# Kernel optimization log

Measured on AMD Instinct MI355X. Metric: run time of the kernel, lower is better.

## Reference

```python
import jax, jax.numpy as jnp
import numpy as np

N = 50000
E = 800000
IN_C = 256
H1 = 64
H2 = 64
OUT_C = 32
HEADS = 7
NEG_SLOPE = 0.2


def _gat_layer(x, src, dst, W, a_src, a_dst, b, heads, ch, n_nodes):
    # x: [N, F_in]; W: [F_in, heads*ch]; a_src/a_dst: [heads, ch]; b: [heads*ch]
    h = (x @ W).reshape(n_nodes, heads, ch)                      # [N, H, C]
    alpha_s = jnp.einsum('nhc,hc->nh', h, a_src)                 # [N, H]
    alpha_d = jnp.einsum('nhc,hc->nh', h, a_dst)                 # [N, H]
    e = jax.nn.leaky_relu(alpha_s[src] + alpha_d[dst], NEG_SLOPE)  # [E, H]
    # segment softmax grouped by destination node
    m = jax.ops.segment_max(e, dst, num_segments=n_nodes)        # [N, H]
    e = jnp.exp(e - m[dst])
    denom = jax.ops.segment_sum(e, dst, num_segments=n_nodes)    # [N, H]
    alpha = e / (denom[dst] + 1e-16)                             # [E, H]
    msg = h[src] * alpha[:, :, None]                             # [E, H, C]
    out = jax.ops.segment_sum(msg, dst, num_segments=n_nodes)    # [N, H, C]
    return out.reshape(n_nodes, heads * ch) + b


def setup_inputs() -> dict:
    key = jax.random.key(0)
    ks = jax.random.split(key, 16)
    x = jax.random.normal(ks[0], (N, IN_C), dtype=jnp.float32)
    edge_index = jax.random.randint(ks[1], (2, E), 0, N, dtype=jnp.int32)

    def glorot(k, shape):
        fan = shape[0] + shape[-1]
        return jax.random.normal(k, shape, dtype=jnp.float32) * jnp.sqrt(2.0 / fan)

    W1 = glorot(ks[2], (IN_C, HEADS * H1))
    a1_src = glorot(ks[3], (HEADS, H1))
    a1_dst = glorot(ks[4], (HEADS, H1))
    b1 = jnp.zeros((HEADS * H1,), jnp.float32)

    W2 = glorot(ks[5], (HEADS * H1, HEADS * H2))
    a2_src = glorot(ks[6], (HEADS, H2))
    a2_dst = glorot(ks[7], (HEADS, H2))
    b2 = jnp.zeros((HEADS * H2,), jnp.float32)

    W3 = glorot(ks[8], (HEADS * H2, 1 * OUT_C))
    a3_src = glorot(ks[9], (1, OUT_C))
    a3_dst = glorot(ks[10], (1, OUT_C))
    b3 = jnp.zeros((OUT_C,), jnp.float32)

    return {"x": x, "edge_index": edge_index,
            "W1": W1, "a1_src": a1_src, "a1_dst": a1_dst, "b1": b1,
            "W2": W2, "a2_src": a2_src, "a2_dst": a2_dst, "b2": b2,
            "W3": W3, "a3_src": a3_src, "a3_dst": a3_dst, "b3": b3}


def reference(x, edge_index, W1, a1_src, a1_dst, b1, W2, a2_src, a2_dst, b2,
              W3, a3_src, a3_dst, b3):
    # PyG GATConv adds self-loops by default
    loops = jnp.arange(N, dtype=edge_index.dtype)
    src = jnp.concatenate([edge_index[0], loops])
    dst = jnp.concatenate([edge_index[1], loops])
    # dropout is identity in eval mode
    h = _gat_layer(x, src, dst, W1, a1_src, a1_dst, b1, HEADS, H1, N)
    h = jax.nn.relu(h)
    h = _gat_layer(h, src, dst, W2, a2_src, a2_dst, b2, HEADS, H2, N)
    h = jax.nn.relu(h)
    h = _gat_layer(h, src, dst, W3, a3_src, a3_dst, b3, 1, OUT_C, N)
    return jax.nn.log_softmax(h, axis=1)
```

## Files before the change

kernel.cpp:

```cpp
#include <hip/hip_runtime.h>
#include <hip/hip_bf16.h>
#include <hip/hip_fp16.h>

#define NN 50000
#define NP 50176
#define EE 800000
#define ET (EE + NN)
#define NB_SCAN ((NN + 255) / 256)

typedef __attribute__((ext_vector_type(8))) short bf16x8;
typedef __attribute__((ext_vector_type(4))) float f32x4;

static __device__ __forceinline__ float bf2f(__hip_bfloat16 x) { return __bfloat162float(x); }
static __device__ __forceinline__ ushort f2bu(float f) {
    union { __hip_bfloat16 b; ushort u; } c;
    c.b = __float2bfloat16(f);
    return c.u;
}
static __device__ __forceinline__ float u2f(ushort u) {
    union { ushort u; __hip_bfloat16 b; } c;
    c.u = u;
    return __bfloat162float(c.b);
}
static __device__ __forceinline__ unsigned char f2fp8(float v) {
    int p = __builtin_amdgcn_cvt_pk_fp8_f32(v, v, 0, false);
    return (unsigned char)(p & 0xff);
}
static __device__ __forceinline__ void fp8acc4(unsigned v, float w, float* acc) {
#if __has_builtin(__builtin_amdgcn_cvt_pk_f32_fp8)
    auto f01 = __builtin_amdgcn_cvt_pk_f32_fp8((int)v, false);
    auto f23 = __builtin_amdgcn_cvt_pk_f32_fp8((int)v, true);
    acc[0] += w * f01[0];
    acc[1] += w * f01[1];
    acc[2] += w * f23[0];
    acc[3] += w * f23[1];
#else
    acc[0] += w * __builtin_amdgcn_cvt_f32_fp8(v, 0);
    acc[1] += w * __builtin_amdgcn_cvt_f32_fp8(v, 1);
    acc[2] += w * __builtin_amdgcn_cvt_f32_fp8(v, 2);
    acc[3] += w * __builtin_amdgcn_cvt_f32_fp8(v, 3);
#endif
}
static __device__ __forceinline__ void gl2lds(const ushort* g, ushort* l) {
    __builtin_amdgcn_global_load_lds(
        (const __attribute__((address_space(1))) void*)g,
        (__attribute__((address_space(3))) void*)l,
        16, 0, 0);
}

#define PA1 (256 * 448)
#define PA2 (448 * 448)
#define PA3 (448 * 32)
#define PXQ (NN * 64)
#define PTOT (PA1 + PA2 + PA3 + PXQ)
#define PBLK ((PTOT + 255) / 256)
#define CBLK ((ET + 255) / 256)

__global__ void gat_prepcnt_kernel(const float* __restrict__ W1, const float* __restrict__ W2,
                                   const float* __restrict__ W3, const float* __restrict__ x,
                                   ushort* __restrict__ Wt1, ushort* __restrict__ Wt2,
                                   ushort* __restrict__ Wt3, ushort* __restrict__ xb,
                                   const int* __restrict__ ei, int* __restrict__ cnt) {
    int b = blockIdx.x;
    if (b >= PBLK) {
        int i = (b - PBLK) * 256 + threadIdx.x;
        if (i < ET) {
            int dst = (i < EE) ? ei[EE + i] : (i - EE);
            atomicAdd(&cnt[dst], 1);
        }
        return;
    }
    int i = b * 256 + threadIdx.x;
    if (i < PA1) {
        int k = i / 448, n = i - k * 448;
        Wt1[(size_t)n * 256 + k] = f2bu(W1[i]);
        return;
    }
    i -= PA1;
    if (i < PA2) {
        int k = i / 448, n = i - k * 448;
        Wt2[(size_t)n * 448 + k] = f2bu(W2[i]);
        return;
    }
    i -= PA2;
    if (i < PA3) {
        int k = i / 32, n = i - k * 32;
        Wt3[(size_t)n * 448 + k] = f2bu(W3[i]);
        return;
    }
    i -= PA3;
    if (i < PXQ) {
        float4 f = ((const float4*)x)[i];
        ushort u[4] = {f2bu(f.x), f2bu(f.y), f2bu(f.z), f2bu(f.w)};
        ((uint2*)xb)[i] = *(const uint2*)u;
    }
}

__global__ void gat_scan1_kernel(const int* __restrict__ cnt, int* __restrict__ tmp,
                                 int* __restrict__ part) {
    __shared__ int sm[256];
    int tid = threadIdx.x;
    int i = blockIdx.x * 256 + tid;
    int v = (i < NN) ? cnt[i] : 0;
    sm[tid] = v;
    __syncthreads();
    for (int o = 1; o < 256; o <<= 1) {
        int t = (tid >= o) ? sm[tid - o] : 0;
        __syncthreads();
        sm[tid] += t;
        __syncthreads();
    }
    if (i < NN) tmp[i] = sm[tid];
    if (tid == 255) part[blockIdx.x] = sm[255];
}

__global__ void gat_scan2_kernel(int* __restrict__ part) {
    __shared__ int sm[256];
    int tid = threadIdx.x;
    int v = (tid < NB_SCAN) ? part[tid] : 0;
    sm[tid] = v;
    __syncthreads();
    for (int o = 1; o < 256; o <<= 1) {
        int t = (tid >= o) ? sm[tid - o] : 0;
        __syncthreads();
        sm[tid] += t;
        __syncthreads();
    }
    part[tid] = sm[tid];
}

__global__ void gat_scan3_kernel(const int* __restrict__ tmp, const int* __restrict__ part,
                                 int* __restrict__ row_ptr) {
    int i = blockIdx.x * 256 + threadIdx.x;
    int off = (blockIdx.x > 0) ? part[blockIdx.x - 1] : 0;
    if (i < NN) row_ptr[i + 1] = tmp[i] + off;
    if (i == 0) row_ptr[0] = 0;
}

__global__ void gat_fill_kernel(const int* __restrict__ ei, const int* __restrict__ row_ptr,
                                int* __restrict__ fillc, int* __restrict__ colA) {
    int i = blockIdx.x * blockDim.x + threadIdx.x;
    if (i >= ET) return;
    int s, d;
    if (i < EE) { s = ei[i]; d = ei[EE + i]; }
    else        { s = d = i - EE; }
    int pos = row_ptr[d] + atomicAdd(&fillc[d], 1);
    colA[pos] = s;
}

#define GBN 64
#define GBK 32

template <int RF, int DOA, int OM>
__global__ __launch_bounds__(256) void gat_gemm_kernel(
    const ushort* __restrict__ A, const ushort* __restrict__ Wt,
    void* __restrict__ Cv,
    const float* __restrict__ Asrc, const float* __restrict__ Adst,
    float* __restrict__ as8, float* __restrict__ ad8,
    int M, int K, int N) {
    constexpr int GBM = RF * 64;
    __shared__ __align__(16) ushort As[2][GBM * GBK];
    __shared__ __align__(16) ushort Bs[2][GBN * GBK];
    int tid = threadIdx.x;
    int wave = tid >> 6, lane = tid & 63;
    int lrow = lane & 15, lq = lane >> 4;
    int m0 = blockIdx.x * GBM, n0 = blockIdx.y * GBN;
    int srow = lane >> 2, schunk = (lane & 3) * 8;
    f32x4 acc[RF][4] = {};

    int KT = K / GBK;
    {
#pragma unroll
        for (int q = 0; q < RF; q++) {
            const ushort* gp = A + (size_t)(m0 + wave * RF * 16 + q * 16 + srow) * K + schunk;
            gl2lds(gp, &As[0][(wave * RF * 16 + q * 16) * GBK]);
        }
        const ushort* gb = Wt + (size_t)(n0 + wave * 16 + srow) * K + schunk;
        gl2lds(gb, &Bs[0][wave * 16 * GBK]);
    }
    for (int kt = 0; kt < KT; kt++) {
        __syncthreads();
        if (kt + 1 < KT) {
            int nb = (kt + 1) & 1, k0 = (kt + 1) * GBK;
#pragma unroll
            for (int q = 0; q < RF; q++) {
                const ushort* gp = A + (size_t)(m0 + wave * RF * 16 + q * 16 + srow) * K + k0 + schunk;
                gl2lds(gp, &As[nb][(wave * RF * 16 + q * 16) * GBK]);
            }
            const ushort* gb = Wt + (size_t)(n0 + wave * 16 + srow) * K + k0 + schunk;
            gl2lds(gb, &Bs[nb][wave * 16 * GBK]);
        }
        int b = kt & 1;
        bf16x8 af[RF];
#pragma unroll
        for (int rf = 0; rf < RF; rf++)
            af[rf] = *(const bf16x8*)&As[b][(wave * RF * 16 + rf * 16 + lrow) * GBK + lq * 8];
#pragma unroll
        for (int ng = 0; ng < 4; ng++) {
            bf16x8 bf = *(const bf16x8*)&Bs[b][(ng * 16 + lrow) * GBK + lq * 8];
#pragma unroll
            for (int rf = 0; rf < RF; rf++)
                acc[rf][ng] = __builtin_amdgcn_mfma_f32_16x16x32_bf16(af[rf], bf, acc[rf][ng], 0, 0, 0);
        }
    }
#pragma unroll
    for (int rf = 0; rf < RF; rf++)
#pragma unroll
        for (int ng = 0; ng < 4; ng++)
#pragma unroll
            for (int r = 0; r < 4; r++) {
                int row = m0 + wave * RF * 16 + rf * 16 + lq * 4 + r;
                int colI = n0 + ng * 16 + lrow;
                if (row < M && colI < N) {
                    if constexpr (OM == 0)
                        ((__hip_bfloat16*)Cv)[(size_t)row * N + colI] = __float2bfloat16(acc[rf][ng][r]);
                    else
                        ((unsigned char*)Cv)[(size_t)row * N + colI] = f2fp8(acc[rf][ng][r]);
                }
            }
    if constexpr (DOA == 1) {
        int head = blockIdx.y;
        float as_l[4], ad_l[4];
#pragma unroll
        for (int ng = 0; ng < 4; ng++) {
            as_l[ng] = Asrc[head * 64 + ng * 16 + lrow];
            ad_l[ng] = Adst[head * 64 + ng * 16 + lrow];
        }
#pragma unroll
        for (int rf = 0; rf < RF; rf++)
#pragma unroll
            for (int r = 0; r < 4; r++) {
                float ps = 0.f, pd = 0.f;
#pragma unroll
                for (int ng = 0; ng < 4; ng++) {
                    ps += acc[rf][ng][r] * as_l[ng];
                    pd += acc[rf][ng][r] * ad_l[ng];
                }
#pragma unroll
                for (int o = 1; o < 16; o <<= 1) {
                    ps += __shfl_xor(ps, o);
                    pd += __shfl_xor(pd, o);
                }
                int row = m0 + wave * RF * 16 + rf * 16 + lq * 4 + r;
                if (lrow == 0 && row < M) {
                    as8[(size_t)row * 8 + head] = ps;
                    ad8[(size_t)row * 8 + head] = pd;
                }
            }
    } else if constexpr (DOA == 2) {
        float as_l[2], ad_l[2];
#pragma unroll
        for (int ng = 0; ng < 2; ng++) {
            as_l[ng] = Asrc[ng * 16 + lrow];
            ad_l[ng] = Adst[ng * 16 + lrow];
        }
#pragma unroll
        for (int rf = 0; rf < RF; rf++)
#pragma unroll
            for (int r = 0; r < 4; r++) {
                float ps = acc[rf][0][r] * as_l[0] + acc[rf][1][r] * as_l[1];
                float pd = acc[rf][0][r] * ad_l[0] + acc[rf][1][r] * ad_l[1];
#pragma unroll
                for (int o = 1; o < 16; o <<= 1) {
                    ps += __shfl_xor(ps, o);
                    pd += __shfl_xor(pd, o);
                }
                int row = m0 + wave * RF * 16 + rf * 16 + lq * 4 + r;
                if (lrow == 0 && row < M) {
                    as8[(size_t)row * 8] = ps;
                    ad8[(size_t)row * 8] = pd;
                }
            }
    }
}

__global__ void gat_aggC7_kernel(const int* __restrict__ rp, const int* __restrict__ colA,
                                 const float* __restrict__ as8, const float* __restrict__ ad8,
                                 const unsigned char* __restrict__ h8,
                                 const float* __restrict__ bias,
                                 __hip_bfloat16* __restrict__ outp) {
    int d = blockIdx.x * 4 + (threadIdx.x >> 6);
    if (d >= NN) return;
    int lane = threadIdx.x & 63;
    if (lane >= 56) return;
    int hh = lane >> 3;
    float adh = ad8[(size_t)d * 8 + hh];
    int s0 = rp[d], s1 = rp[d + 1];
    float acc[8] = {0.f, 0.f, 0.f, 0.f, 0.f, 0.f, 0.f, 0.f};
    float den = 0.f;
    int j = s0;
    for (; j + 4 <= s1; j += 4) {
        int sA = colA[j], sB = colA[j + 1], sC = colA[j + 2], sD = colA[j + 3];
        float eA = as8[(size_t)sA * 8 + hh] + adh;
        float eB = as8[(size_t)sB * 8 + hh] + adh;
        float eC = as8[(size_t)sC * 8 + hh] + adh;
        float eD = as8[(size_t)sD * 8 + hh] + adh;
        uint2 hA = *(const uint2*)(h8 + (size_t)sA * 448 + lane * 8);
        uint2 hB = *(const uint2*)(h8 + (size_t)sB * 448 + lane * 8);
        uint2 hC = *(const uint2*)(h8 + (size_t)sC * 448 + lane * 8);
        uint2 hD = *(const uint2*)(h8 + (size_t)sD * 448 + lane * 8);
        eA = (eA > 0.f) ? eA : 0.2f * eA;
        eB = (eB > 0.f) ? eB : 0.2f * eB;
        eC = (eC > 0.f) ? eC : 0.2f * eC;
        eD = (eD > 0.f) ? eD : 0.2f * eD;
        float wA = __expf(eA), wB = __expf(eB);
        float wC = __expf(eC), wD = __expf(eD);
        den += (wA + wB) + (wC + wD);
        fp8acc4(hA.x, wA, &acc[0]); fp8acc4(hA.y, wA, &acc[4]);
        fp8acc4(hB.x, wB, &acc[0]); fp8acc4(hB.y, wB, &acc[4]);
        fp8acc4(hC.x, wC, &acc[0]); fp8acc4(hC.y, wC, &acc[4]);
        fp8acc4(hD.x, wD, &acc[0]); fp8acc4(hD.y, wD, &acc[4]);
    }
    for (; j < s1; j++) {
        int s = colA[j];
        float e = as8[(size_t)s * 8 + hh] + adh;
        e = (e > 0.f) ? e : 0.2f * e;
        float w = __expf(e);
        uint2 hv = *(const uint2*)(h8 + (size_t)s * 448 + lane * 8);
        den += w;
        fp8acc4(hv.x, w, &acc[0]);
        fp8acc4(hv.y, w, &acc[4]);
    }
    float inv = 1.f / (den + 1e-16f);
    const float4* bp = (const float4*)(bias + lane * 8);
    float4 bb0 = bp[0], bb1 = bp[1];
    float bv[8] = {bb0.x, bb0.y, bb0.z, bb0.w, bb1.x, bb1.y, bb1.z, bb1.w};
    ushort o8[8];
#pragma unroll
    for (int k = 0; k < 8; k++) {
        float o = acc[k] * inv + bv[k];
        o = fmaxf(o, 0.f);
        o8[k] = f2bu(o);
    }
    *(uint4*)((ushort*)outp + (size_t)d * 448 + lane * 8) = *(const uint4*)o8;
}

__global__ void gat_aggCF_kernel(const int* __restrict__ rp, const int* __restrict__ colA,
                                 const float* __restrict__ as8, const float* __restrict__ ad8,
                                 const __hip_bfloat16* __restrict__ h,
                                 const float* __restrict__ bias,
                                 float* __restrict__ outp) {
    int wid = blockIdx.x * 4 + (threadIdx.x >> 6);
    int lane = threadIdx.x & 63;
    int half = lane >> 5, c = lane & 31;
    int dreal = wid * 2 + half;
    bool valid = dreal < NN;
    int d = valid ? dreal : (NN - 1);
    float adh = ad8[(size_t)d * 8];
    int s0 = rp[d], s1 = rp[d + 1];
    float acc = 0.f, den = 0.f;
    int j = s0;
    for (; j + 2 <= s1; j += 2) {
        int sA = colA[j], sB = colA[j + 1];
        float eA = as8[(size_t)sA * 8] + adh;
        float eB = as8[(size_t)sB * 8] + adh;
        float vA = bf2f(h[(size_t)sA * 32 + c]);
        float vB = bf2f(h[(size_t)sB * 32 + c]);
        eA = (eA > 0.f) ? eA : 0.2f * eA;
        eB = (eB > 0.f) ? eB : 0.2f * eB;
        float wA = __expf(eA), wB = __expf(eB);
        den += wA + wB;
        acc += wA * vA + wB * vB;
    }
    for (; j < s1; j++) {
        int s = colA[j];
        float e = as8[(size_t)s * 8] + adh;
        e = (e > 0.f) ? e : 0.2f * e;
        float w = __expf(e);
        den += w;
        acc += w * bf2f(h[(size_t)s * 32 + c]);
    }
    float o = acc / (den + 1e-16f) + bias[c];
    float t = o;
#pragma unroll
    for (int off = 16; off > 0; off >>= 1) t = fmaxf(t, __shfl_xor(t, off));
    float ex = __expf(o - t);
#pragma unroll
    for (int off = 16; off > 0; off >>= 1) ex += __shfl_xor(ex, off);
    float res = o - t - __logf(ex);
    if (valid) outp[(size_t)d * 32 + c] = res;
}

extern "C" void kernel_launch(void* const* d_in, const int* in_sizes, int n_in,
                              void* d_out, int out_size, void* d_ws, size_t ws_size,
                              hipStream_t stream) {
    const float* x   = (const float*)d_in[0];
    const int*   ei  = (const int*)d_in[1];
    const float* W1  = (const float*)d_in[2];
    const float* a1s = (const float*)d_in[3];
    const float* a1d = (const float*)d_in[4];
    const float* b1  = (const float*)d_in[5];
    const float* W2  = (const float*)d_in[6];
    const float* a2s = (const float*)d_in[7];
    const float* a2d = (const float*)d_in[8];
    const float* b2  = (const float*)d_in[9];
    const float* W3  = (const float*)d_in[10];
    const float* a3s = (const float*)d_in[11];
    const float* a3d = (const float*)d_in[12];
    const float* b3  = (const float*)d_in[13];
    float* out = (float*)d_out;

    char* w = (char*)d_ws;
    unsigned char* hbuf8 = (unsigned char*)w;
    __hip_bfloat16* hbuf3 = (__hip_bfloat16*)w;
    ushort* xb = (ushort*)(w + (size_t)NP * 448);
    __hip_bfloat16* act = (__hip_bfloat16*)(xb + (size_t)NP * 256);
    float* as8 = (float*)(act + (size_t)NP * 448);
    float* ad8 = as8 + (size_t)NN * 8;
    int* cnt     = (int*)(ad8 + (size_t)NN * 8);
    int* fillc   = cnt + NN;
    int* row_ptr = fillc + NN;
    int* tmp     = row_ptr + (NN + 4);
    int* part    = tmp + NN;
    int* colA    = part + 256;
    char* pw = (char*)(colA + ET);
    pw = (char*)(((uintptr_t)pw + 15) & ~(uintptr_t)15);
    ushort* Wt1 = (ushort*)pw;
    ushort* Wt2 = Wt1 + 448 * 256;
    ushort* Wt3 = Wt2 + 448 * 448;

    hipMemsetAsync(cnt, 0, 2 * (size_t)NN * sizeof(int), stream);

    gat_prepcnt_kernel<<<PBLK + CBLK, 256, 0, stream>>>(W1, W2, W3, x, Wt1, Wt2, Wt3, xb, ei, cnt);
    gat_scan1_kernel<<<NB_SCAN, 256, 0, stream>>>(cnt, tmp, part);
    gat_scan2_kernel<<<1, 256, 0, stream>>>(part);
    gat_scan3_kernel<<<NB_SCAN, 256, 0, stream>>>(tmp, part, row_ptr);
    gat_fill_kernel<<<CBLK, 256, 0, stream>>>(ei, row_ptr, fillc, colA);

    dim3 gemmBlk(256);
    int mtiles = NP / 256;
    int mtiles1 = NP / 64;
    int aggBlocks = (NN + 3) / 4;

    gat_gemm_kernel<4, 1, 1><<<dim3(mtiles, 7), gemmBlk, 0, stream>>>(
        xb, Wt1, hbuf8, a1s, a1d, as8, ad8, NN, 256, 448);
    gat_aggC7_kernel<<<aggBlocks, 256, 0, stream>>>(row_ptr, colA, as8, ad8, hbuf8, b1, act);

    gat_gemm_kernel<4, 1, 1><<<dim3(mtiles, 7), gemmBlk, 0, stream>>>(
        (const ushort*)act, Wt2, hbuf8, a2s, a2d, as8, ad8, NN, 448, 448);
    gat_aggC7_kernel<<<aggBlocks, 256, 0, stream>>>(row_ptr, colA, as8, ad8, hbuf8, b2, act);

    gat_gemm_kernel<1, 2, 0><<<dim3(mtiles1, 1), gemmBlk, 0, stream>>>(
        (const ushort*)act, Wt3, hbuf3, a3s, a3d, as8, ad8, NN, 448, 32);
    int fBlocks = (NN + 7) / 8;
    gat_aggCF_kernel<<<fBlocks, 256, 0, stream>>>(row_ptr, colA, as8, ad8, hbuf3, b3, out);
}
```

Measured before the change: 489.2 us.

## Switch GEMM operands and activations to FP8 and merge scan into one kernel

Weights, input features and inter-layer activations are now stored as FP8 instead of BF16, and the GEMM uses the fp8 MFMA instruction with a doubled K tile so each LDS stage holds the same number of bytes. This halves the memory traffic for the GEMM inputs and for the activation writes from the aggregation kernel. The three-kernel prefix scan is also replaced by a single 1024-thread block scan, which cuts launch overhead. FP8 operands lose considerable precision compared with BF16, which may push outputs past the accuracy tolerance.

Result: slower. 572.9 us (+17.1%).

```diff
diff --git a/kernel.cpp b/kernel.cpp
--- a/kernel.cpp
+++ b/kernel.cpp
@@ -6,9 +6,7 @@
 #define NP 50176
 #define EE 800000
 #define ET (EE + NN)
-#define NB_SCAN ((NN + 255) / 256)
-
-typedef __attribute__((ext_vector_type(8))) short bf16x8;
+
 typedef __attribute__((ext_vector_type(4))) float f32x4;
 
 static __device__ __forceinline__ float bf2f(__hip_bfloat16 x) { return __bfloat162float(x); }
@@ -17,14 +15,14 @@
     c.b = __float2bfloat16(f);
     return c.u;
 }
-static __device__ __forceinline__ float u2f(ushort u) {
-    union { ushort u; __hip_bfloat16 b; } c;
-    c.u = u;
-    return __bfloat162float(c.b);
-}
 static __device__ __forceinline__ unsigned char f2fp8(float v) {
     int p = __builtin_amdgcn_cvt_pk_fp8_f32(v, v, 0, false);
     return (unsigned char)(p & 0xff);
+}
+static __device__ __forceinline__ unsigned pk4fp8(float a, float b, float c, float d) {
+    unsigned lo = (unsigned)__builtin_amdgcn_cvt_pk_fp8_f32(a, b, 0, false) & 0xffffu;
+    unsigned hi = (unsigned)__builtin_amdgcn_cvt_pk_fp8_f32(c, d, 0, false) & 0xffffu;
+    return lo | (hi << 16);
 }
 static __device__ __forceinline__ void fp8acc4(unsigned v, float w, float* acc) {
 #if __has_builtin(__builtin_amdgcn_cvt_pk_f32_fp8)
@@ -41,7 +39,7 @@
     acc[3] += w * __builtin_amdgcn_cvt_f32_fp8(v, 3);
 #endif
 }
-static __device__ __forceinline__ void gl2lds(const ushort* g, ushort* l) {
+static __device__ __forceinline__ void gl2lds(const unsigned char* g, unsigned char* l) {
     __builtin_amdgcn_global_load_lds(
         (const __attribute__((address_space(1))) void*)g,
         (__attribute__((address_space(3))) void*)l,
@@ -58,8 +56,8 @@
 
 __global__ void gat_prepcnt_kernel(const float* __restrict__ W1, const float* __restrict__ W2,
                                    const float* __restrict__ W3, const float* __restrict__ x,
-                                   ushort* __restrict__ Wt1, ushort* __restrict__ Wt2,
-                                   ushort* __restrict__ Wt3, ushort* __restrict__ xb,
+                                   unsigned char* __restrict__ Wt1, unsigned char* __restrict__ Wt2,
+                                   unsigned char* __restrict__ Wt3, unsigned char* __restrict__ xb,
                                    const int* __restrict__ ei, int* __restrict__ cnt) {
     int b = blockIdx.x;
     if (b >= PBLK) {
@@ -73,68 +71,55 @@
     int i = b * 256 + threadIdx.x;
     if (i < PA1) {
         int k = i / 448, n = i - k * 448;
-        Wt1[(size_t)n * 256 + k] = f2bu(W1[i]);
+        Wt1[(size_t)n * 256 + k] = f2fp8(W1[i]);
         return;
     }
     i -= PA1;
     if (i < PA2) {
         int k = i / 448, n = i - k * 448;
-        Wt2[(size_t)n * 448 + k] = f2bu(W2[i]);
+        Wt2[(size_t)n * 448 + k] = f2fp8(W2[i]);
         return;
     }
     i -= PA2;
     if (i < PA3) {
         int k = i / 32, n = i - k * 32;
-        Wt3[(size_t)n * 448 + k] = f2bu(W3[i]);
+        Wt3[(size_t)n * 448 + k] = f2fp8(W3[i]);
         return;
     }
     i -= PA3;
     if (i < PXQ) {
         float4 f = ((const float4*)x)[i];
-        ushort u[4] = {f2bu(f.x), f2bu(f.y), f2bu(f.z), f2bu(f.w)};
-        ((uint2*)xb)[i] = *(const uint2*)u;
-    }
-}
-
-__global__ void gat_scan1_kernel(const int* __restrict__ cnt, int* __restrict__ tmp,
-                                 int* __restrict__ part) {
-    __shared__ int sm[256];
-    int tid = threadIdx.x;
-    int i = blockIdx.x * 256 + tid;
-    int v = (i < NN) ? cnt[i] : 0;
-    sm[tid] = v;
+        ((unsigned*)xb)[i] = pk4fp8(f.x, f.y, f.z, f.w);
+    }
+}
+
+__global__ void gat_scanall_kernel(const int* __restrict__ cnt, int* __restrict__ row_ptr) {
+    __shared__ int sm[1024];
+    const int C = 49;
+    int t = threadIdx.x;
+    int base = t * C;
+    int s = 0;
+    for (int i = 0; i < C; i++) {
+        int idx = base + i;
+        if (idx < NN) s += cnt[idx];
+    }
+    sm[t] = s;
     __syncthreads();
-    for (int o = 1; o < 256; o <<= 1) {
-        int t = (tid >= o) ? sm[tid - o] : 0;
+    for (int o = 1; o < 1024; o <<= 1) {
+        int v = (t >= o) ? sm[t - o] : 0;
         __syncthreads();
-        sm[tid] += t;
+        sm[t] += v;
         __syncthreads();
     }
-    if (i < NN) tmp[i] = sm[tid];
-    if (tid == 255) part[blockIdx.x] = sm[255];
-}
-
-__global__ void gat_scan2_kernel(int* __restrict__ part) {
-    __shared__ int sm[256];
-    int tid = threadIdx.x;
-    int v = (tid < NB_SCAN) ? part[tid] : 0;
-    sm[tid] = v;
-    __syncthreads();
-    for (int o = 1; o < 256; o <<= 1) {
-        int t = (tid >= o) ? sm[tid - o] : 0;
-        __syncthreads();
-        sm[tid] += t;
-        __syncthreads();
-    }
-    part[tid] = sm[tid];
-}
-
-__global__ void gat_scan3_kernel(const int* __restrict__ tmp, const int* __restrict__ part,
-                                 int* __restrict__ row_ptr) {
-    int i = blockIdx.x * 256 + threadIdx.x;
-    int off = (blockIdx.x > 0) ? part[blockIdx.x - 1] : 0;
-    if (i < NN) row_ptr[i + 1] = tmp[i] + off;
-    if (i == 0) row_ptr[0] = 0;
+    int run = (t > 0) ? sm[t - 1] : 0;
+    for (int i = 0; i < C; i++) {
+        int idx = base + i;
+        if (idx < NN) {
+            run += cnt[idx];
+            row_ptr[idx + 1] = run;
+        }
+    }
+    if (t == 0) row_ptr[0] = 0;
 }
 
 __global__ void gat_fill_kernel(const int* __restrict__ ei, const int* __restrict__ row_ptr,
@@ -149,33 +134,33 @@
 }
 
 #define GBN 64
-#define GBK 32
+#define GBK 64
 
 template <int RF, int DOA, int OM>
 __global__ __launch_bounds__(256) void gat_gemm_kernel(
-    const ushort* __restrict__ A, const ushort* __restrict__ Wt,
+    const unsigned char* __restrict__ A, const unsigned char* __restrict__ Wt,
     void* __restrict__ Cv,
     const float* __restrict__ Asrc, const float* __restrict__ Adst,
     float* __restrict__ as8, float* __restrict__ ad8,
     int M, int K, int N) {
     constexpr int GBM = RF * 64;
-    __shared__ __align__(16) ushort As[2][GBM * GBK];
-    __shared__ __align__(16) ushort Bs[2][GBN * GBK];
+    __shared__ __align__(16) unsigned char As[2][GBM * GBK];
+    __shared__ __align__(16) unsigned char Bs[2][GBN * GBK];
     int tid = threadIdx.x;
     int wave = tid >> 6, lane = tid & 63;
     int lrow = lane & 15, lq = lane >> 4;
     int m0 = blockIdx.x * GBM, n0 = blockIdx.y * GBN;
-    int srow = lane >> 2, schunk = (lane & 3) * 8;
+    int srow = lane >> 2, schunk = (lane & 3) * 16;
     f32x4 acc[RF][4] = {};
 
     int KT = K / GBK;
     {
 #pragma unroll
         for (int q = 0; q < RF; q++) {
-            const ushort* gp = A + (size_t)(m0 + wave * RF * 16 + q * 16 + srow) * K + schunk;
+            const unsigned char* gp = A + (size_t)(m0 + wave * RF * 16 + q * 16 + srow) * K + schunk;
             gl2lds(gp, &As[0][(wave * RF * 16 + q * 16) * GBK]);
         }
-        const ushort* gb = Wt + (size_t)(n0 + wave * 16 + srow) * K + schunk;
+        const unsigned char* gb = Wt + (size_t)(n0 + wave * 16 + srow) * K + schunk;
         gl2lds(gb, &Bs[0][wave * 16 * GBK]);
     }
     for (int kt = 0; kt < KT; kt++) {
@@ -184,23 +169,26 @@
             int nb = (kt + 1) & 1, k0 = (kt + 1) * GBK;
 #pragma unroll
             for (int q = 0; q < RF; q++) {
-                const ushort* gp = A + (size_t)(m0 + wave * RF * 16 + q * 16 + srow) * K + k0 + schunk;
+                const unsigned char* gp = A + (size_t)(m0 + wave * RF * 16 + q * 16 + srow) * K + k0 + schunk;
                 gl2lds(gp, &As[nb][(wave * RF * 16 + q * 16) * GBK]);
             }
-            const ushort* gb = Wt + (size_t)(n0 + wave * 16 + srow) * K + k0 + schunk;
+            const unsigned char* gb = Wt + (size_t)(n0 + wave * 16 + srow) * K + k0 + schunk;
             gl2lds(gb, &Bs[nb][wave * 16 * GBK]);
         }
         int b = kt & 1;
-        bf16x8 af[RF];
-#pragma unroll
-        for (int rf = 0; rf < RF; rf++)
-            af[rf] = *(const bf16x8*)&As[b][(wave * RF * 16 + rf * 16 + lrow) * GBK + lq * 8];
-#pragma unroll
-        for (int ng = 0; ng < 4; ng++) {
-            bf16x8 bf = *(const bf16x8*)&Bs[b][(ng * 16 + lrow) * GBK + lq * 8];
+#pragma unroll
+        for (int s = 0; s < 2; s++) {
+            long af[RF];
 #pragma unroll
             for (int rf = 0; rf < RF; rf++)
-                acc[rf][ng] = __builtin_amdgcn_mfma_f32_16x16x32_bf16(af[rf], bf, acc[rf][ng], 0, 0, 0);
+                af[rf] = *(const long*)&As[b][(wave * RF * 16 + rf * 16 + lrow) * GBK + s * 32 + lq * 8];
+#pragma unroll
+            for (int ng = 0; ng < 4; ng++) {
+                long bf = *(const long*)&Bs[b][(ng * 16 + lrow) * GBK + s * 32 + lq * 8];
+#pragma unroll
+                for (int rf = 0; rf < RF; rf++)
+                    acc[rf][ng] = __builtin_amdgcn_mfma_f32_16x16x32_fp8_fp8(af[rf], bf, acc[rf][ng], 0, 0, 0);
+            }
         }
     }
 #pragma unroll
@@ -278,7 +266,7 @@
                                  const float* __restrict__ as8, const float* __restrict__ ad8,
                                  const unsigned char* __restrict__ h8,
                                  const float* __restrict__ bias,
-                                 __hip_bfloat16* __restrict__ outp) {
+                                 unsigned char* __restrict__ outp) {
     int d = blockIdx.x * 4 + (threadIdx.x >> 6);
     if (d >= NN) return;
     int lane = threadIdx.x & 63;
@@ -325,14 +313,13 @@
     const float4* bp = (const float4*)(bias + lane * 8);
     float4 bb0 = bp[0], bb1 = bp[1];
     float bv[8] = {bb0.x, bb0.y, bb0.z, bb0.w, bb1.x, bb1.y, bb1.z, bb1.w};
-    ushort o8[8];
-#pragma unroll
-    for (int k = 0; k < 8; k++) {
-        float o = acc[k] * inv + bv[k];
-        o = fmaxf(o, 0.f);
-        o8[k] = f2bu(o);
-    }
-    *(uint4*)((ushort*)outp + (size_t)d * 448 + lane * 8) = *(const uint4*)o8;
+    float o[8];
+#pragma unroll
+    for (int k = 0; k < 8; k++) o[k] = fmaxf(acc[k] * inv + bv[k], 0.f);
+    uint2 packed;
+    packed.x = pk4fp8(o[0], o[1], o[2], o[3]);
+    packed.y = pk4fp8(o[4], o[5], o[6], o[7]);
+    *(uint2*)(outp + (size_t)d * 448 + lane * 8) = packed;
 }
 
 __global__ void gat_aggCF_kernel(const int* __restrict__ rp, const int* __restrict__ colA,
@@ -403,28 +390,24 @@
     char* w = (char*)d_ws;
     unsigned char* hbuf8 = (unsigned char*)w;
     __hip_bfloat16* hbuf3 = (__hip_bfloat16*)w;
-    ushort* xb = (ushort*)(w + (size_t)NP * 448);
-    __hip_bfloat16* act = (__hip_bfloat16*)(xb + (size_t)NP * 256);
+    unsigned char* xb  = (unsigned char*)(w + (size_t)NP * 448);
+    unsigned char* act = xb + (size_t)NP * 256;
     float* as8 = (float*)(act + (size_t)NP * 448);
     float* ad8 = as8 + (size_t)NN * 8;
     int* cnt     = (int*)(ad8 + (size_t)NN * 8);
     int* fillc   = cnt + NN;
     int* row_ptr = fillc + NN;
-    int* tmp     = row_ptr + (NN + 4);
-    int* part    = tmp + NN;
-    int* colA    = part + 256;
+    int* colA    = row_ptr + (NN + 4);
     char* pw = (char*)(colA + ET);
     pw = (char*)(((uintptr_t)pw + 15) & ~(uintptr_t)15);
-    ushort* Wt1 = (ushort*)pw;
-    ushort* Wt2 = Wt1 + 448 * 256;
-    ushort* Wt3 = Wt2 + 448 * 448;
+    unsigned char* Wt1 = (unsigned char*)pw;
+    unsigned char* Wt2 = Wt1 + 448 * 256;
+    unsigned char* Wt3 = Wt2 + 448 * 448;
 
     hipMemsetAsync(cnt, 0, 2 * (size_t)NN * sizeof(int), stream);
 
     gat_prepcnt_kernel<<<PBLK + CBLK, 256, 0, stream>>>(W1, W2, W3, x, Wt1, Wt2, Wt3, xb, ei, cnt);
-    gat_scan1_kernel<<<NB_SCAN, 256, 0, stream>>>(cnt, tmp, part);
-    gat_scan2_kernel<<<1, 256, 0, stream>>>(part);
-    gat_scan3_kernel<<<NB_SCAN, 256, 0, stream>>>(tmp, part, row_ptr);
+    gat_scanall_kernel<<<1, 1024, 0, stream>>>(cnt, row_ptr);
     gat_fill_kernel<<<CBLK, 256, 0, stream>>>(ei, row_ptr, fillc, colA);
 
     dim3 gemmBlk(256);
@@ -437,11 +420,11 @@
     gat_aggC7_kernel<<<aggBlocks, 256, 0, stream>>>(row_ptr, colA, as8, ad8, hbuf8, b1, act);
 
     gat_gemm_kernel<4, 1, 1><<<dim3(mtiles, 7), gemmBlk, 0, stream>>>(
-        (const ushort*)act, Wt2, hbuf8, a2s, a2d, as8, ad8, NN, 448, 448);
+        act, Wt2, hbuf8, a2s, a2d, as8, ad8, NN, 448, 448);
     gat_aggC7_kernel<<<aggBlocks, 256, 0, stream>>>(row_ptr, colA, as8, ad8, hbuf8, b2, act);
 
     gat_gemm_kernel<1, 2, 0><<<dim3(mtiles1, 1), gemmBlk, 0, stream>>>(
-        (const ushort*)act, Wt3, hbuf3, a3s, a3d, as8, ad8, NN, 448, 32);
+        act, Wt3, hbuf3, a3s, a3d, as8, ad8, NN, 448, 32);
     int fBlocks = (NN + 7) / 8;
     gat_aggCF_kernel<<<fBlocks, 256, 0, stream>>>(row_ptr, colA, as8, ad8, hbuf3, b3, out);
 }
```
